# Kernel tuning notes

Measured on AMD Instinct MI355X. Metric: run time of the kernel, lower is better.

Reference implementation:

```python
import jax, jax.numpy as jnp
import numpy as np

ALPHA = 0.25
GAMMA = 2.0
VAR = jnp.array([0.1, 0.1, 0.2, 0.2, 0.1, 0.1, 0.2, 0.2], dtype=jnp.float32)


def calc_iou(a, b):
    # a: [A,4] anchors, b: [M,4] gt boxes -> IoU [A,M]
    area = (b[:, 2] - b[:, 0]) * (b[:, 3] - b[:, 1])
    iw = jnp.maximum(jnp.minimum(a[:, 2:3], b[:, 2]) - jnp.maximum(a[:, 0:1], b[:, 0]), 0.0)
    ih = jnp.maximum(jnp.minimum(a[:, 3:4], b[:, 3]) - jnp.maximum(a[:, 1:2], b[:, 1]), 0.0)
    ua = jnp.maximum(((a[:, 2] - a[:, 0]) * (a[:, 3] - a[:, 1]))[:, None] + area - iw * ih, 1e-8)
    return iw * ih / ua


def _per_sample(cls_p, reg, anchor, ann1, ann2):
    A = anchor.shape[0]
    M = ann1.shape[0]
    C = cls_p.shape[1]
    clsp = jnp.clip(cls_p, 1e-4, 1.0 - 1e-4)
    iou = calc_iou(anchor, ann1[:, :4])               # [A,M]
    bto = jnp.max(iou, axis=1)                        # best_truth_overlap [A]
    bti = jnp.argmax(iou, axis=1)                     # best_truth_idx [A]
    bpi = jnp.argmax(iou, axis=0)                     # best_prior_idx [M]
    bto = bto.at[bpi].set(2.0)
    owner = jnp.full((A,), -1, jnp.int32).at[bpi].max(jnp.arange(M, dtype=jnp.int32))
    bti = jnp.where(owner >= 0, owner, bti.astype(jnp.int32))
    pos = bto >= 0.5
    neg = bto < 0.4
    assigned = ann1[bti]                              # [A,6]
    labels = assigned[:, 4].astype(jnp.int32)
    onehot = jax.nn.one_hot(labels, C, dtype=clsp.dtype)
    targets = jnp.where(neg[:, None], 0.0, -1.0)
    targets = jnp.where(pos[:, None], onehot, targets)
    af = jnp.where(targets == 1.0, ALPHA, 1.0 - ALPHA)
    fw = af * jnp.where(targets == 1.0, 1.0 - clsp, clsp) ** GAMMA
    bce = -(targets * jnp.log(clsp) + (1.0 - targets) * jnp.log(1.0 - clsp))
    cls_loss = jnp.where(targets != -1.0, fw * bce, 0.0)
    npos = jnp.sum(pos).astype(clsp.dtype)
    cls_out = cls_loss.sum() / jnp.maximum(npos, 1.0)

    aw = anchor[:, 2] - anchor[:, 0]
    ah = anchor[:, 3] - anchor[:, 1]
    acx = anchor[:, 0] + 0.5 * aw
    acy = anchor[:, 1] + 0.5 * ah
    # track-id first-match between frames (replaces nested python loops)
    match = assigned[:, 5][:, None] == ann2[:, 5][None, :]   # [A,M2]
    has = jnp.any(match, axis=1)
    first = jnp.argmax(match, axis=1)
    ann_next = jnp.where(has[:, None], ann2[first], 0.0)     # [A,6]
    gw0 = assigned[:, 2] - assigned[:, 0]
    gh0 = assigned[:, 3] - assigned[:, 1]
    gcx = assigned[:, 0] + 0.5 * gw0
    gcy = assigned[:, 1] + 0.5 * gh0
    gw = jnp.maximum(gw0, 1.0)
    gh = jnp.maximum(gh0, 1.0)
    nw0 = ann_next[:, 2] - ann_next[:, 0]
    nh0 = ann_next[:, 3] - ann_next[:, 1]
    ncx = ann_next[:, 0] + 0.5 * nw0
    ncy = ann_next[:, 1] + 0.5 * nh0
    nw = jnp.maximum(nw0, 1.0)
    nh = jnp.maximum(nh0, 1.0)
    t = jnp.stack([
        (gcx - acx) / aw, (gcy - acy) / ah, jnp.log(gw / aw), jnp.log(gh / ah),
        (ncx - acx) / aw, (ncy - acy) / ah, jnp.log(nw / aw), jnp.log(nh / ah)
    ], axis=1) / VAR                                          # [A,8]
    reg_mask = jnp.concatenate([
        jnp.ones((A, 4), clsp.dtype),
        jnp.broadcast_to(has[:, None], (A, 4)).astype(clsp.dtype)
    ], axis=1)
    diff = jnp.abs(t - reg) * reg_mask
    hub = jnp.where(diff <= 1.0 / 9.0, 0.5 * 9.0 * diff ** 2, diff - 0.5 / 9.0)
    reg_out = jnp.sum(hub * pos[:, None].astype(clsp.dtype)) / jnp.maximum(npos * 8.0, 1.0)
    return cls_out, reg_out


def reference(classifications, regressions, anchors, annotations1, annotations2):
    cl, rl = jax.vmap(_per_sample, in_axes=(0, 0, None, 0, 0))(
        classifications, regressions, anchors[0], annotations1, annotations2)
    return jnp.mean(cl, keepdims=True), jnp.mean(rl, keepdims=True)


def setup_inputs() -> dict:
    key = jax.random.key(0)
    ks = jax.random.split(key, 10)
    B, A, C, M = 8, 100000, 80, 32
    IMG = 512.0

    def rand_boxes(k, prefix):
        k1, k2 = jax.random.split(k)
        ctr = jax.random.uniform(k1, prefix + (2,), jnp.float32, 0.0, IMG)
        wh = jax.random.uniform(k2, prefix + (2,), jnp.float32, 16.0, 128.0)
        return jnp.concatenate([ctr - 0.5 * wh, ctr + 0.5 * wh], axis=-1)

    anchors = rand_boxes(ks[0], (1, A))
    classifications = jax.random.uniform(ks[1], (B, A, C), jnp.float32)
    regressions = jax.random.normal(ks[2], (B, A, 8), jnp.float32) * 0.1

    def make_ann(kb, ki):
        boxes = rand_boxes(kb, (B, M))
        lbl = jax.random.randint(ki, (B, M, 1), 0, C).astype(jnp.float32)
        tid = jax.random.randint(jax.random.fold_in(ki, 1), (B, M, 1), 0, 40).astype(jnp.float32)
        return jnp.concatenate([boxes, lbl, tid], axis=-1)

    annotations1 = make_ann(ks[3], ks[4])
    annotations2 = make_ann(ks[5], ks[6])
    return {"classifications": classifications, "regressions": regressions,
            "anchors": anchors, "annotations1": annotations1, "annotations2": annotations2}
```

## Files before the change

kernel.cpp:

```cpp
#include <hip/hip_runtime.h>

typedef unsigned long long ull;

#define MMAX 64

__global__ void k_iou(const float* __restrict__ anchors, const float* __restrict__ ann1,
                      float* __restrict__ bto, int* __restrict__ bti, int* __restrict__ acode,
                      ull* __restrict__ part_key, int* __restrict__ part_cnt,
                      int A, int M, int NBLK) {
    __shared__ float s_box[MMAX][4];
    __shared__ float s_area[MMAX];
    __shared__ float s_lab[MMAX];
    __shared__ ull s_part[4][MMAX];
    __shared__ int s_cnt[4];
    const int b = blockIdx.y;
    const int blk = blockIdx.x;
    const int tid = threadIdx.x;
    for (int i = tid; i < M; i += blockDim.x) {
        const float* g = ann1 + ((size_t)b * M + i) * 6;
        float x1 = g[0], y1 = g[1], x2 = g[2], y2 = g[3];
        s_box[i][0] = x1; s_box[i][1] = y1; s_box[i][2] = x2; s_box[i][3] = y2;
        s_area[i] = (x2 - x1) * (y2 - y1);
        s_lab[i] = g[4];
    }
    __syncthreads();

    const int base = blk * (blockDim.x * 4);
    float ax1[4], ay1[4], ax2[4], ay2[4], aar[4];
    int aidx[4]; bool val[4];
#pragma unroll
    for (int u = 0; u < 4; ++u) {
        int a = base + u * blockDim.x + tid;
        aidx[u] = a; val[u] = (a < A);
        float4 av = make_float4(0.f, 0.f, 0.f, 0.f);
        if (val[u]) av = ((const float4*)anchors)[a];
        ax1[u] = av.x; ay1[u] = av.y; ax2[u] = av.z; ay2[u] = av.w;
        aar[u] = (av.z - av.x) * (av.w - av.y);
    }
    float best[4] = {-1.f, -1.f, -1.f, -1.f};
    int bestj[4] = {0, 0, 0, 0};
    const int lane = tid & 63, wid = tid >> 6;

    for (int j = 0; j < M; ++j) {
        float bx1 = s_box[j][0], by1 = s_box[j][1], bx2 = s_box[j][2], by2 = s_box[j][3];
        float bar = s_area[j];
        ull key = 0ull;
#pragma unroll
        for (int u = 0; u < 4; ++u) {
            float iw = fmaxf(fminf(ax2[u], bx2) - fmaxf(ax1[u], bx1), 0.f);
            float ih = fmaxf(fminf(ay2[u], by2) - fmaxf(ay1[u], by1), 0.f);
            float inter = iw * ih;
            float ua = fmaxf(aar[u] + bar - inter, 1e-8f);
            float iou = inter / ua;
            if (val[u]) {
                if (iou > best[u]) { best[u] = iou; bestj[u] = j; }
                ull k2 = (((ull)__float_as_uint(iou)) << 32) | (ull)(0xFFFFFFFFu - (unsigned)aidx[u]);
                if (k2 > key) key = k2;
            }
        }
#pragma unroll
        for (int off = 32; off > 0; off >>= 1) {
            ull o = __shfl_down(key, off);
            if (o > key) key = o;
        }
        if (lane == 0) s_part[wid][j] = key;
    }
    int cnt = 0;
#pragma unroll
    for (int u = 0; u < 4; ++u) {
        if (val[u]) {
            float bv = best[u];
            bto[(size_t)b * A + aidx[u]] = bv;
            bti[(size_t)b * A + aidx[u]] = bestj[u];
            int code;
            if (bv >= 0.5f) { code = (int)s_lab[bestj[u]]; ++cnt; }
            else code = (bv < 0.4f) ? -1 : -2;
            acode[(size_t)b * A + aidx[u]] = code;
        }
    }
#pragma unroll
    for (int off = 32; off > 0; off >>= 1) cnt += __shfl_down(cnt, off);
    if (lane == 0) s_cnt[wid] = cnt;
    __syncthreads();
    if (tid < M) {
        ull key = s_part[0][tid];
        if (s_part[1][tid] > key) key = s_part[1][tid];
        if (s_part[2][tid] > key) key = s_part[2][tid];
        if (s_part[3][tid] > key) key = s_part[3][tid];
        part_key[((size_t)b * NBLK + blk) * M + tid] = key;
    }
    if (tid == 0) part_cnt[b * NBLK + blk] = s_cnt[0] + s_cnt[1] + s_cnt[2] + s_cnt[3];
}

__global__ void k_assign(const ull* __restrict__ part_key, const int* __restrict__ part_cnt,
                         const float* __restrict__ ann1,
                         float* __restrict__ bto, int* __restrict__ bti, int* __restrict__ acode,
                         int* __restrict__ npos, float* __restrict__ out,
                         int A, int M, int NBLK) {
    const int b = blockIdx.x;
    const int tid = threadIdx.x;
    __shared__ int s_a[MMAX];
    if (tid < M) {
        ull key = 0ull;
        for (int k = 0; k < NBLK; ++k) {
            ull v = part_key[((size_t)b * NBLK + k) * M + tid];
            if (v > key) key = v;
        }
        s_a[tid] = (int)(0xFFFFFFFFu - (unsigned)(key & 0xFFFFFFFFull));
    }
    __syncthreads();
    int corr = 0;
    if (tid < M) {
        int a = s_a[tid];
        bool owner = true;
        for (int j2 = tid + 1; j2 < M; ++j2)
            if (s_a[j2] == a) owner = false;
        if (owner) {
            float pre = bto[(size_t)b * A + a];
            bto[(size_t)b * A + a] = 2.0f;
            bti[(size_t)b * A + a] = tid;
            acode[(size_t)b * A + a] = (int)ann1[((size_t)b * M + tid) * 6 + 4];
            if (pre < 0.5f) corr = 1;
        }
    }
    int cnt = corr;
    for (int k = tid; k < NBLK; k += 64) cnt += part_cnt[b * NBLK + k];
#pragma unroll
    for (int off = 32; off > 0; off >>= 1) cnt += __shfl_down(cnt, off);
    if (tid == 0) npos[b] = cnt;
    if (b == 0 && tid == 0) { out[0] = 0.f; out[1] = 0.f; }
}

__device__ __forceinline__ float bg_term(float x) {
    float p = fminf(fmaxf(x, 1e-4f), 1.0f - 1e-4f);
    return p * p * (-__logf(1.0f - p));
}

template <int C4C>
__global__ __launch_bounds__(256, 4)
void k_cls(const float* __restrict__ cls, const int* __restrict__ acode,
           const int* __restrict__ npos, float* __restrict__ out,
           int A, int c4_rt, float invB) {
    const int c4 = (C4C > 0) ? C4C : c4_rt;
    const int b = blockIdx.y;
    const int tid = threadIdx.x;
    const int N4 = A * c4;
    const float4* cb = (const float4*)(cls + (size_t)b * A * (c4 * 4));
    const int* ac = acode + (size_t)b * A;
    float lsum = 0.f;
    const int stride = gridDim.x * blockDim.x;
    int i = blockIdx.x * blockDim.x + tid;

    for (; i + 3 * stride < N4; i += 4 * stride) {
        int idx[4], code[4];
        float4 x[4];
#pragma unroll
        for (int u = 0; u < 4; ++u) { idx[u] = i + u * stride; code[u] = ac[idx[u] / c4]; }
#pragma unroll
        for (int u = 0; u < 4; ++u) x[u] = cb[idx[u]];
#pragma unroll
        for (int u = 0; u < 4; ++u) {
            float tmp = bg_term(x[u].x) + bg_term(x[u].y) + bg_term(x[u].z) + bg_term(x[u].w);
            float w = (code[u] == -2) ? 0.f : 0.75f;
            lsum = fmaf(w, tmp, lsum);
            int c0 = (idx[u] - (idx[u] / c4) * c4) * 4;
            int rel = code[u] - c0;
            if (((unsigned)rel) < 4u) {
                float xs = (rel == 0) ? x[u].x : (rel == 1) ? x[u].y : (rel == 2) ? x[u].z : x[u].w;
                float p = fminf(fmaxf(xs, 1e-4f), 1.0f - 1e-4f);
                float q = 1.f - p;
                lsum -= 0.75f * p * p * (-__logf(q));
                lsum += 0.25f * q * q * (-__logf(p));
            }
        }
    }
    for (; i < N4; i += stride) {
        int code = ac[i / c4];
        float4 x = cb[i];
        float tmp = bg_term(x.x) + bg_term(x.y) + bg_term(x.z) + bg_term(x.w);
        float w = (code == -2) ? 0.f : 0.75f;
        lsum = fmaf(w, tmp, lsum);
        int c0 = (i - (i / c4) * c4) * 4;
        int rel = code - c0;
        if (((unsigned)rel) < 4u) {
            float xs = (rel == 0) ? x.x : (rel == 1) ? x.y : (rel == 2) ? x.z : x.w;
            float p = fminf(fmaxf(xs, 1e-4f), 1.0f - 1e-4f);
            float q = 1.f - p;
            lsum -= 0.75f * p * p * (-__logf(q));
            lsum += 0.25f * q * q * (-__logf(p));
        }
    }
#pragma unroll
    for (int off = 32; off > 0; off >>= 1) lsum += __shfl_down(lsum, off);
    __shared__ float s_l[4];
    if ((tid & 63) == 0) s_l[tid >> 6] = lsum;
    __syncthreads();
    if (tid == 0) {
        float np_ = (float)npos[b];
        atomicAdd(&out[0], (s_l[0] + s_l[1] + s_l[2] + s_l[3]) / fmaxf(np_, 1.f) * invB);
    }
}

__global__ void k_reg(const float* __restrict__ anchors, const float* __restrict__ ann1,
                      const float* __restrict__ ann2, const float* __restrict__ regs,
                      const float* __restrict__ bto, const int* __restrict__ bti,
                      const int* __restrict__ npos, float* __restrict__ out,
                      int A, int M, int M2, float invB) {
    __shared__ float s_a1[MMAX * 6];
    __shared__ float s_a2[MMAX * 6];
    const int b = blockIdx.y;
    const int tid = threadIdx.x;
    for (int i = tid; i < M * 6; i += blockDim.x) s_a1[i] = ann1[(size_t)b * M * 6 + i];
    for (int i = tid; i < M2 * 6; i += blockDim.x) s_a2[i] = ann2[(size_t)b * M2 * 6 + i];
    __syncthreads();

    const int a = blockIdx.x * blockDim.x + tid;
    float sum = 0.f;
    if (a < A) {
        float v = bto[(size_t)b * A + a];
        if (v >= 0.5f) {
            const int ji = bti[(size_t)b * A + a];
            const float* as = &s_a1[ji * 6];
            float4 av = ((const float4*)anchors)[a];
            float aw = av.z - av.x, ah = av.w - av.y;
            float acx = av.x + 0.5f * aw, acy = av.y + 0.5f * ah;
            float gw0 = as[2] - as[0], gh0 = as[3] - as[1];
            float gcx = as[0] + 0.5f * gw0, gcy = as[1] + 0.5f * gh0;
            float gw = fmaxf(gw0, 1.f), gh = fmaxf(gh0, 1.f);
            float t[8];
            t[0] = ((gcx - acx) / aw) / 0.1f;
            t[1] = ((gcy - acy) / ah) / 0.1f;
            t[2] = __logf(gw / aw) / 0.2f;
            t[3] = __logf(gh / ah) / 0.2f;
            int nterm = 4;
            float tid5 = as[5];
            int first = -1;
            for (int j2 = 0; j2 < M2; ++j2) {
                if (s_a2[j2 * 6 + 5] == tid5) { first = j2; break; }
            }
            if (first >= 0) {
                const float* ns = &s_a2[first * 6];
                float nw0 = ns[2] - ns[0], nh0 = ns[3] - ns[1];
                float ncx = ns[0] + 0.5f * nw0, ncy = ns[1] + 0.5f * nh0;
                float nw = fmaxf(nw0, 1.f), nh = fmaxf(nh0, 1.f);
                t[4] = ((ncx - acx) / aw) / 0.1f;
                t[5] = ((ncy - acy) / ah) / 0.1f;
                t[6] = __logf(nw / aw) / 0.2f;
                t[7] = __logf(nh / ah) / 0.2f;
                nterm = 8;
            }
            const float* rg = regs + ((size_t)b * A + a) * 8;
            for (int k = 0; k < nterm; ++k) {
                float d = fabsf(t[k] - rg[k]);
                sum += (d <= (1.0f / 9.0f)) ? (4.5f * d * d) : (d - (0.5f / 9.0f));
            }
        }
    }
#pragma unroll
    for (int off = 32; off > 0; off >>= 1) sum += __shfl_down(sum, off);
    __shared__ float s_rs[4];
    if ((tid & 63) == 0) s_rs[tid >> 6] = sum;
    __syncthreads();
    if (tid == 0) {
        float s = s_rs[0] + s_rs[1] + s_rs[2] + s_rs[3];
        if (s != 0.f) {
            float np_ = (float)npos[b];
            atomicAdd(&out[1], s / fmaxf(np_ * 8.f, 1.f) * invB);
        }
    }
}

extern "C" void kernel_launch(void* const* d_in, const int* in_sizes, int n_in,
                              void* d_out, int out_size, void* d_ws, size_t ws_size,
                              hipStream_t stream) {
    const float* cls = (const float*)d_in[0];
    const float* regs = (const float*)d_in[1];
    const float* anchors = (const float*)d_in[2];
    const float* ann1 = (const float*)d_in[3];
    const float* ann2 = (const float*)d_in[4];
    float* out = (float*)d_out;

    const int A = in_sizes[2] / 4;
    const int B = in_sizes[1] / (A * 8);
    const int C = in_sizes[0] / (B * A);
    const int M = in_sizes[3] / (B * 6);
    const int M2 = in_sizes[4] / (B * 6);
    const int NBLK = (A + 1023) / 1024;

    char* ws = (char*)d_ws;
    size_t off = 0;
    float* bto = (float*)(ws + off);     off += (size_t)B * A * sizeof(float);        off = (off + 255) & ~(size_t)255;
    int* bti = (int*)(ws + off);         off += (size_t)B * A * sizeof(int);          off = (off + 255) & ~(size_t)255;
    int* acode = (int*)(ws + off);       off += (size_t)B * A * sizeof(int);          off = (off + 255) & ~(size_t)255;
    ull* part_key = (ull*)(ws + off);    off += (size_t)B * NBLK * M * sizeof(ull);   off = (off + 255) & ~(size_t)255;
    int* part_cnt = (int*)(ws + off);    off += (size_t)B * NBLK * sizeof(int);       off = (off + 255) & ~(size_t)255;
    int* npos = (int*)(ws + off);        off += (size_t)B * sizeof(int);

    dim3 g1(NBLK, B);
    k_iou<<<g1, dim3(256), 0, stream>>>(anchors, ann1, bto, bti, acode, part_key, part_cnt, A, M, NBLK);

    k_assign<<<dim3(B), dim3(64), 0, stream>>>(part_key, part_cnt, ann1, bto, bti, acode, npos, out, A, M, NBLK);

    dim3 g3(512, B);
    const float invB = 1.0f / (float)B;
    if (C == 80)
        k_cls<20><<<g3, dim3(256), 0, stream>>>(cls, acode, npos, out, A, C / 4, invB);
    else
        k_cls<0><<<g3, dim3(256), 0, stream>>>(cls, acode, npos, out, A, C / 4, invB);

    dim3 g4((A + 255) / 256, B);
    k_reg<<<g4, dim3(256), 0, stream>>>(anchors, ann1, ann2, regs, bto, bti, npos, out, A, M, M2, invB);
}
```

Before: 480.9 us.

## Move positive-class correction to regression kernel, precompute float weights for cls pass

The classification kernel no longer handles the positive-label correction term per element. It now reads a precomputed per-anchor float weight array (written in the IoU and assign kernels) and runs an 8-way unrolled loop with a higher occupancy launch bound. The sparse positive-anchor correction is computed in the regression kernel by gathering the single labeled logit. This removes integer division, modulo and branching from the bandwidth-bound hot loop, at the cost of an extra workspace array and an extra scattered read and atomic per block in the regression kernel.

Result: slower. 528.2 us (+9.8%).

```diff
diff --git a/kernel.cpp b/kernel.cpp
--- a/kernel.cpp
+++ b/kernel.cpp
@@ -6,6 +6,7 @@
 
 __global__ void k_iou(const float* __restrict__ anchors, const float* __restrict__ ann1,
                       float* __restrict__ bto, int* __restrict__ bti, int* __restrict__ acode,
+                      float* __restrict__ wf,
                       ull* __restrict__ part_key, int* __restrict__ part_cnt,
                       int A, int M, int NBLK) {
     __shared__ float s_box[MMAX][4];
@@ -76,6 +77,7 @@
             if (bv >= 0.5f) { code = (int)s_lab[bestj[u]]; ++cnt; }
             else code = (bv < 0.4f) ? -1 : -2;
             acode[(size_t)b * A + aidx[u]] = code;
+            wf[(size_t)b * A + aidx[u]] = (code == -2) ? 0.f : 0.75f;
         }
     }
 #pragma unroll
@@ -95,6 +97,7 @@
 __global__ void k_assign(const ull* __restrict__ part_key, const int* __restrict__ part_cnt,
                          const float* __restrict__ ann1,
                          float* __restrict__ bto, int* __restrict__ bti, int* __restrict__ acode,
+                         float* __restrict__ wf,
                          int* __restrict__ npos, float* __restrict__ out,
                          int A, int M, int NBLK) {
     const int b = blockIdx.x;
@@ -120,6 +123,7 @@
             bto[(size_t)b * A + a] = 2.0f;
             bti[(size_t)b * A + a] = tid;
             acode[(size_t)b * A + a] = (int)ann1[((size_t)b * M + tid) * 6 + 4];
+            wf[(size_t)b * A + a] = 0.75f;
             if (pre < 0.5f) corr = 1;
         }
     }
@@ -137,8 +141,8 @@
 }
 
 template <int C4C>
-__global__ __launch_bounds__(256, 4)
-void k_cls(const float* __restrict__ cls, const int* __restrict__ acode,
+__global__ __launch_bounds__(256, 8)
+void k_cls(const float* __restrict__ cls, const float* __restrict__ wf,
            const int* __restrict__ npos, float* __restrict__ out,
            int A, int c4_rt, float invB) {
     const int c4 = (C4C > 0) ? C4C : c4_rt;
@@ -146,49 +150,29 @@
     const int tid = threadIdx.x;
     const int N4 = A * c4;
     const float4* cb = (const float4*)(cls + (size_t)b * A * (c4 * 4));
-    const int* ac = acode + (size_t)b * A;
+    const float* wb = wf + (size_t)b * A;
     float lsum = 0.f;
     const int stride = gridDim.x * blockDim.x;
     int i = blockIdx.x * blockDim.x + tid;
 
-    for (; i + 3 * stride < N4; i += 4 * stride) {
-        int idx[4], code[4];
-        float4 x[4];
-#pragma unroll
-        for (int u = 0; u < 4; ++u) { idx[u] = i + u * stride; code[u] = ac[idx[u] / c4]; }
-#pragma unroll
-        for (int u = 0; u < 4; ++u) x[u] = cb[idx[u]];
-#pragma unroll
-        for (int u = 0; u < 4; ++u) {
+    for (; i + 7 * stride < N4; i += 8 * stride) {
+        float w[8];
+        float4 x[8];
+#pragma unroll
+        for (int u = 0; u < 8; ++u) w[u] = wb[(i + u * stride) / c4];
+#pragma unroll
+        for (int u = 0; u < 8; ++u) x[u] = cb[i + u * stride];
+#pragma unroll
+        for (int u = 0; u < 8; ++u) {
             float tmp = bg_term(x[u].x) + bg_term(x[u].y) + bg_term(x[u].z) + bg_term(x[u].w);
-            float w = (code[u] == -2) ? 0.f : 0.75f;
-            lsum = fmaf(w, tmp, lsum);
-            int c0 = (idx[u] - (idx[u] / c4) * c4) * 4;
-            int rel = code[u] - c0;
-            if (((unsigned)rel) < 4u) {
-                float xs = (rel == 0) ? x[u].x : (rel == 1) ? x[u].y : (rel == 2) ? x[u].z : x[u].w;
-                float p = fminf(fmaxf(xs, 1e-4f), 1.0f - 1e-4f);
-                float q = 1.f - p;
-                lsum -= 0.75f * p * p * (-__logf(q));
-                lsum += 0.25f * q * q * (-__logf(p));
-            }
+            lsum = fmaf(w[u], tmp, lsum);
         }
     }
     for (; i < N4; i += stride) {
-        int code = ac[i / c4];
+        float w = wb[i / c4];
         float4 x = cb[i];
         float tmp = bg_term(x.x) + bg_term(x.y) + bg_term(x.z) + bg_term(x.w);
-        float w = (code == -2) ? 0.f : 0.75f;
         lsum = fmaf(w, tmp, lsum);
-        int c0 = (i - (i / c4) * c4) * 4;
-        int rel = code - c0;
-        if (((unsigned)rel) < 4u) {
-            float xs = (rel == 0) ? x.x : (rel == 1) ? x.y : (rel == 2) ? x.z : x.w;
-            float p = fminf(fmaxf(xs, 1e-4f), 1.0f - 1e-4f);
-            float q = 1.f - p;
-            lsum -= 0.75f * p * p * (-__logf(q));
-            lsum += 0.25f * q * q * (-__logf(p));
-        }
     }
 #pragma unroll
     for (int off = 32; off > 0; off >>= 1) lsum += __shfl_down(lsum, off);
@@ -203,9 +187,11 @@
 
 __global__ void k_reg(const float* __restrict__ anchors, const float* __restrict__ ann1,
                       const float* __restrict__ ann2, const float* __restrict__ regs,
+                      const float* __restrict__ cls,
                       const float* __restrict__ bto, const int* __restrict__ bti,
+                      const int* __restrict__ acode,
                       const int* __restrict__ npos, float* __restrict__ out,
-                      int A, int M, int M2, float invB) {
+                      int A, int M, int M2, int C, float invB) {
     __shared__ float s_a1[MMAX * 6];
     __shared__ float s_a2[MMAX * 6];
     const int b = blockIdx.y;
@@ -215,10 +201,16 @@
     __syncthreads();
 
     const int a = blockIdx.x * blockDim.x + tid;
-    float sum = 0.f;
+    float sum = 0.f, csum = 0.f;
     if (a < A) {
         float v = bto[(size_t)b * A + a];
         if (v >= 0.5f) {
+            int label = acode[(size_t)b * A + a];
+            float xs = cls[((size_t)b * A + a) * C + label];
+            float p = fminf(fmaxf(xs, 1e-4f), 1.0f - 1e-4f);
+            float q = 1.f - p;
+            csum = 0.25f * q * q * (-__logf(p)) - 0.75f * p * p * (-__logf(q));
+
             const int ji = bti[(size_t)b * A + a];
             const float* as = &s_a1[ji * 6];
             float4 av = ((const float4*)anchors)[a];
@@ -257,16 +249,19 @@
         }
     }
 #pragma unroll
-    for (int off = 32; off > 0; off >>= 1) sum += __shfl_down(sum, off);
-    __shared__ float s_rs[4];
-    if ((tid & 63) == 0) s_rs[tid >> 6] = sum;
+    for (int off = 32; off > 0; off >>= 1) {
+        sum += __shfl_down(sum, off);
+        csum += __shfl_down(csum, off);
+    }
+    __shared__ float s_rs[4], s_cs[4];
+    if ((tid & 63) == 0) { s_rs[tid >> 6] = sum; s_cs[tid >> 6] = csum; }
     __syncthreads();
     if (tid == 0) {
         float s = s_rs[0] + s_rs[1] + s_rs[2] + s_rs[3];
-        if (s != 0.f) {
-            float np_ = (float)npos[b];
-            atomicAdd(&out[1], s / fmaxf(np_ * 8.f, 1.f) * invB);
-        }
+        float c = s_cs[0] + s_cs[1] + s_cs[2] + s_cs[3];
+        float np_ = (float)npos[b];
+        if (s != 0.f) atomicAdd(&out[1], s / fmaxf(np_ * 8.f, 1.f) * invB);
+        if (c != 0.f) atomicAdd(&out[0], c / fmaxf(np_, 1.f) * invB);
     }
 }
 
@@ -292,22 +287,23 @@
     float* bto = (float*)(ws + off);     off += (size_t)B * A * sizeof(float);        off = (off + 255) & ~(size_t)255;
     int* bti = (int*)(ws + off);         off += (size_t)B * A * sizeof(int);          off = (off + 255) & ~(size_t)255;
     int* acode = (int*)(ws + off);       off += (size_t)B * A * sizeof(int);          off = (off + 255) & ~(size_t)255;
+    float* wf = (float*)(ws + off);      off += (size_t)B * A * sizeof(float);        off = (off + 255) & ~(size_t)255;
     ull* part_key = (ull*)(ws + off);    off += (size_t)B * NBLK * M * sizeof(ull);   off = (off + 255) & ~(size_t)255;
     int* part_cnt = (int*)(ws + off);    off += (size_t)B * NBLK * sizeof(int);       off = (off + 255) & ~(size_t)255;
     int* npos = (int*)(ws + off);        off += (size_t)B * sizeof(int);
 
     dim3 g1(NBLK, B);
-    k_iou<<<g1, dim3(256), 0, stream>>>(anchors, ann1, bto, bti, acode, part_key, part_cnt, A, M, NBLK);
-
-    k_assign<<<dim3(B), dim3(64), 0, stream>>>(part_key, part_cnt, ann1, bto, bti, acode, npos, out, A, M, NBLK);
+    k_iou<<<g1, dim3(256), 0, stream>>>(anchors, ann1, bto, bti, acode, wf, part_key, part_cnt, A, M, NBLK);
+
+    k_assign<<<dim3(B), dim3(64), 0, stream>>>(part_key, part_cnt, ann1, bto, bti, acode, wf, npos, out, A, M, NBLK);
 
     dim3 g3(512, B);
     const float invB = 1.0f / (float)B;
     if (C == 80)
-        k_cls<20><<<g3, dim3(256), 0, stream>>>(cls, acode, npos, out, A, C / 4, invB);
+        k_cls<20><<<g3, dim3(256), 0, stream>>>(cls, wf, npos, out, A, C / 4, invB);
     else
-        k_cls<0><<<g3, dim3(256), 0, stream>>>(cls, acode, npos, out, A, C / 4, invB);
+        k_cls<0><<<g3, dim3(256), 0, stream>>>(cls, wf, npos, out, A, C / 4, invB);
 
     dim3 g4((A + 255) / 256, B);
-    k_reg<<<g4, dim3(256), 0, stream>>>(anchors, ann1, ann2, regs, bto, bti, npos, out, A, M, M2, invB);
-}
+    k_reg<<<g4, dim3(256), 0, stream>>>(anchors, ann1, ann2, regs, cls, bto, bti, acode, npos, out, A, M, M2, C, invB);
+}
```
